# Kernel optimization log

Measured on AMD Instinct MI355X. Metric: run time of the kernel, lower is better.

The kernel has to match this reference:

```python
import jax, jax.numpy as jnp
import numpy as np

N_NODES = 50000
N_EDGES = 800000
N_GRAPHS = 8
BN_EPS = 1e-5


def setup_inputs() -> dict:
    key = jax.random.key(0)
    ks = iter(jax.random.split(key, 40))
    d = {}
    d["x"] = jax.random.normal(next(ks), (N_NODES, 3), dtype=jnp.float32)
    d["edge_index"] = jax.random.randint(next(ks), (2, N_EDGES), 0, N_NODES, dtype=jnp.int32)
    d["batch"] = jnp.sort(jax.random.randint(next(ks), (N_NODES,), 0, N_GRAPHS, dtype=jnp.int32))
    conv_in = [3, 64, 128]  # dense concat widths feeding each GCN layer
    for i, cin in enumerate(conv_in):
        d[f"W{i}"] = jax.random.normal(next(ks), (cin, 64), dtype=jnp.float32) * (1.0 / np.sqrt(cin))
        d[f"b{i}"] = jax.random.normal(next(ks), (64,), dtype=jnp.float32) * 0.05
        d[f"g{i}"] = jax.random.uniform(next(ks), (64,), dtype=jnp.float32) + 0.5
        d[f"beta{i}"] = jax.random.normal(next(ks), (64,), dtype=jnp.float32) * 0.05
        d[f"rm{i}"] = jax.random.normal(next(ks), (64,), dtype=jnp.float32) * 0.05
        d[f"rv{i}"] = jax.random.uniform(next(ks), (64,), dtype=jnp.float32) + 0.5
    def lin(k, i, o):
        return (jax.random.normal(k, (i, o), dtype=jnp.float32) * (1.0 / np.sqrt(i)),)
    d["enc_w0"], = lin(next(ks), 256, 128); d["enc_b0"] = jax.random.normal(next(ks), (128,), jnp.float32) * 0.05
    d["enc_w1"], = lin(next(ks), 128, 64); d["enc_b1"] = jax.random.normal(next(ks), (64,), jnp.float32) * 0.05
    d["dec_w0"], = lin(next(ks), 64, 32); d["dec_b0"] = jax.random.normal(next(ks), (32,), jnp.float32) * 0.05
    d["dec_w1"], = lin(next(ks), 32, 1); d["dec_b1"] = jax.random.normal(next(ks), (1,), jnp.float32) * 0.05
    return d


def reference(x, edge_index, batch,
              W0, b0, g0, beta0, rm0, rv0,
              W1, b1, g1, beta1, rm1, rv1,
              W2, b2, g2, beta2, rm2, rv2,
              enc_w0, enc_b0, enc_w1, enc_b1,
              dec_w0, dec_b0, dec_w1, dec_b1):
    N = x.shape[0]
    loops = jnp.arange(N, dtype=edge_index.dtype)
    src = jnp.concatenate([edge_index[0], loops])  # GCNConv adds self loops
    dst = jnp.concatenate([edge_index[1], loops])
    deg = jax.ops.segment_sum(jnp.ones_like(src, dtype=x.dtype), dst, num_segments=N)
    dinv = jnp.where(deg > 0, jax.lax.rsqrt(deg), 0.0)
    coef = (dinv[src] * dinv[dst])[:, None]  # symmetric normalization per edge

    def conv_bn_relu(h, W, b, g, beta, rm, rv):
        hw = h @ W                                    # [N, 64]
        out = jax.ops.segment_sum(hw[src] * coef, dst, num_segments=N) + b
        out = (out - rm) * (g * jax.lax.rsqrt(rv + BN_EPS)) + beta  # BN eval mode
        return jax.nn.relu(out)

    params = [(W0, b0, g0, beta0, rm0, rv0),
              (W1, b1, g1, beta1, rm1, rv1),
              (W2, b2, g2, beta2, rm2, rv2)]
    prev = []
    h = x
    for p in params:  # dense connectivity: concat all previous concat-outputs
        h = conv_bn_relu(h, *p)
        h = jnp.concatenate(prev + [h], axis=1)
        prev.append(h)

    e = jax.nn.relu(jax.nn.relu(h @ enc_w0 + enc_b0) @ enc_w1 + enc_b1)  # [N, 64]
    counts = jax.ops.segment_sum(jnp.ones((N,), x.dtype), batch, num_segments=N_GRAPHS)
    gfeat = jax.ops.segment_sum(e, batch, num_segments=N_GRAPHS) / jnp.maximum(counts, 1.0)[:, None]
    out = jax.nn.relu(gfeat @ dec_w0 + dec_b0) @ dec_w1 + dec_b1  # [G, 1]
    return out[:, 0]  # torch.squeeze(output, 1) since num_classes == 1
```

## Files before the change

kernel.cpp:

```cpp
#include <hip/hip_runtime.h>
#include <hip/hip_fp16.h>

#define NN 50000
#define NE 800000
#define NG 8
#define BN_EPS 1e-5f
#define NBLK ((NN + 255) / 256)
#define NPART 8
#define HLD 192

typedef __attribute__((ext_vector_type(8))) short bf16x8;
typedef __attribute__((ext_vector_type(4))) float f32x4;

static __device__ __forceinline__ unsigned short f2bf(float f) {
    unsigned int u = __float_as_uint(f);
    unsigned int r = (u + 0x7FFFu + ((u >> 16) & 1u)) >> 16;
    return (unsigned short)r;
}
static __device__ __forceinline__ float bf2f(unsigned short h) {
    return __uint_as_float((unsigned int)h << 16);
}


__global__ __launch_bounds__(256) void count_deg(const int* __restrict__ dst,
                                                 int* __restrict__ degi) {
    int e = blockIdx.x * 256 + threadIdx.x;
    if (e < NE) atomicAdd(&degi[dst[e]], 1);
}

__global__ __launch_bounds__(256) void scan_partial(const int* __restrict__ degi,
                                                    const float* __restrict__ x,
                                                    int* __restrict__ rowptr,
                                                    int* __restrict__ bsum,
                                                    float* __restrict__ dinv,
                                                    float* __restrict__ xs) {
    __shared__ int sh[256];
    const int tid = threadIdx.x;
    const int i = blockIdx.x * 256 + tid;
    int v = (i < NN) ? degi[i] : 0;
    if (i < NN) {
        float di = rsqrtf((float)(v + 1));
        dinv[i] = di;
        xs[i * 3 + 0] = x[i * 3 + 0] * di;
        xs[i * 3 + 1] = x[i * 3 + 1] * di;
        xs[i * 3 + 2] = x[i * 3 + 2] * di;
    }
    sh[tid] = v;
    __syncthreads();
#pragma unroll
    for (int off = 1; off < 256; off <<= 1) {
        int t = (tid >= off) ? sh[tid - off] : 0;
        __syncthreads();
        sh[tid] += t;
        __syncthreads();
    }
    if (i < NN) rowptr[i] = sh[tid] - v;
    if (tid == 255) bsum[blockIdx.x] = sh[255];
}

__global__ __launch_bounds__(256) void scan_bsums(int* __restrict__ bsum) {
    __shared__ int sh[256];
    const int tid = threadIdx.x;
    int v = (tid < NBLK) ? bsum[tid] : 0;
    sh[tid] = v;
    __syncthreads();
#pragma unroll
    for (int off = 1; off < 256; off <<= 1) {
        int t = (tid >= off) ? sh[tid - off] : 0;
        __syncthreads();
        sh[tid] += t;
        __syncthreads();
    }
    if (tid < NBLK) bsum[tid] = sh[tid] - v;
}

__global__ __launch_bounds__(256) void scan_finalize(const int* __restrict__ bsum,
                                                     int* __restrict__ rowptr,
                                                     int* __restrict__ cursor) {
    const int i = blockIdx.x * 256 + threadIdx.x;
    if (i < NN) {
        int r = rowptr[i] + bsum[blockIdx.x];
        rowptr[i] = r;
        cursor[i] = r;
    }
    if (i == 0) rowptr[NN] = NE;
}

__global__ __launch_bounds__(256) void fill_csr(const int* __restrict__ src,
                                                const int* __restrict__ dst,
                                                int* __restrict__ cursor,
                                                unsigned short* __restrict__ esrc16) {
    int e = blockIdx.x * 256 + threadIdx.x;
    if (e < NE) {
        int s = src[e], d = dst[e];
        int p = atomicAdd(&cursor[d], 1);
        esrc16[p] = (unsigned short)s;
    }
}


static __device__ __forceinline__ void pack_one(const float* W, int NOUT, int li,
                                                float v_override, bool use_override,
                                                unsigned short* ph, unsigned short* pl) {
    int j = li & 7;
    int lane = (li >> 3) & 63;
    int rest = li >> 9;
    int NF = NOUT >> 4;
    int f = rest % NF, ks = rest / NF;
    int k = ks * 32 + (lane >> 4) * 8 + j;
    int col = f * 16 + (lane & 15);
    float v = use_override ? v_override : W[k * NOUT + col];
    unsigned short hi = f2bf(v);
    ph[li] = hi;
    pl[li] = f2bf(v - bf2f(hi));
}

__global__ __launch_bounds__(256) void pack_all(
        const float* __restrict__ W1, const float* __restrict__ W2,
        const float* __restrict__ We0, const float* __restrict__ We1,
        unsigned short* __restrict__ Wp1h, unsigned short* __restrict__ Wp1l,
        unsigned short* __restrict__ Wp2h, unsigned short* __restrict__ Wp2l,
        unsigned short* __restrict__ We0h, unsigned short* __restrict__ We0l,
        unsigned short* __restrict__ We1h, unsigned short* __restrict__ We1l) {
    int idx = blockIdx.x * 256 + threadIdx.x;
    if (idx < 4096) {
        pack_one(W1, 64, idx, 0.f, false, Wp1h, Wp1l);
    } else if (idx < 12288) {
        pack_one(W2, 64, idx - 4096, 0.f, false, Wp2h, Wp2l);
    } else if (idx < 36864) {
        int li = idx - 12288;
        int j = li & 7;
        int lane = (li >> 3) & 63;
        int rest = li >> 9;
        int f = rest % 8, ks = rest / 8;
        int k = ks * 32 + (lane >> 4) * 8 + j;
        int col = f * 16 + (lane & 15);
        float v = (k < 64) ? (We0[k * 128 + col] + We0[(k + 64) * 128 + col])
                           : We0[(k + 64) * 128 + col];
        pack_one(nullptr, 128, li, v, true, We0h, We0l);
    } else if (idx < 45056) {
        pack_one(We1, 64, idx - 36864, 0.f, false, We1h, We1l);
    }
}


template<int K>
__global__ __launch_bounds__(256) void mfma_tab(
        const unsigned short* __restrict__ Ahi,
        const unsigned short* __restrict__ Alo, int lda,
        const unsigned short* __restrict__ Bph,
        const unsigned short* __restrict__ Bpl,
        const float* __restrict__ dinv,
        __half* __restrict__ outH) {
    const int wave = threadIdx.x >> 6;
    const int lane = threadIdx.x & 63;
    const int rbase = blockIdx.x * 64 + wave * 16;
    int arow = rbase + (lane & 15);
    if (arow >= NN) arow = NN - 1;
    const int kbase = (lane >> 4) * 8;

    f32x4 acc[4];
#pragma unroll
    for (int f = 0; f < 4; f++) acc[f] = (f32x4){0.f, 0.f, 0.f, 0.f};

    const unsigned short* pa_hi = Ahi + (size_t)arow * lda + kbase;
    const unsigned short* pa_lo = Alo + (size_t)arow * lda + kbase;
    const unsigned short* pb_hi = Bph + lane * 8;
    const unsigned short* pb_lo = Bpl + lane * 8;

#pragma unroll
    for (int ks = 0; ks < K / 32; ks++) {
        bf16x8 ah = *reinterpret_cast<const bf16x8*>(pa_hi + ks * 32);
        bf16x8 al = *reinterpret_cast<const bf16x8*>(pa_lo + ks * 32);
#pragma unroll
        for (int f = 0; f < 4; f++) {
            bf16x8 bh = *reinterpret_cast<const bf16x8*>(pb_hi + (size_t)((ks * 4 + f) * 64) * 8);
            bf16x8 bl = *reinterpret_cast<const bf16x8*>(pb_lo + (size_t)((ks * 4 + f) * 64) * 8);
            acc[f] = __builtin_amdgcn_mfma_f32_16x16x32_bf16(ah, bh, acc[f], 0, 0, 0);
            acc[f] = __builtin_amdgcn_mfma_f32_16x16x32_bf16(ah, bl, acc[f], 0, 0, 0);
            acc[f] = __builtin_amdgcn_mfma_f32_16x16x32_bf16(al, bh, acc[f], 0, 0, 0);
        }
    }

    const int drow0 = rbase + (lane >> 4) * 4;
    const int dcol = lane & 15;
#pragma unroll
    for (int f = 0; f < 4; f++) {
#pragma unroll
        for (int r = 0; r < 4; r++) {
            int row = drow0 + r;
            if (row < NN)
                outH[(size_t)row * 64 + f * 16 + dcol] = __float2half(acc[f][r] * dinv[row]);
        }
    }
}


__global__ __launch_bounds__(256) void enc_fused(
        const unsigned short* __restrict__ Hhi,
        const unsigned short* __restrict__ Hlo,
        const unsigned short* __restrict__ We0h, const unsigned short* __restrict__ We0l,
        const float* __restrict__ b0,
        const unsigned short* __restrict__ We1h, const unsigned short* __restrict__ We1l,
        const float* __restrict__ b1,
        const int* __restrict__ batch,
        float* __restrict__ gfeat_part) {
    __shared__ float ldsT[4][16][133];
    __shared__ float pool[NG][64];
    const int tid = threadIdx.x;
    const int wave = tid >> 6;
    const int lane = tid & 63;
    const int rbase = blockIdx.x * 64 + wave * 16;

    for (int i = tid; i < NG * 64; i += 256) ((float*)pool)[i] = 0.0f;

    int arow = rbase + (lane & 15);
    if (arow >= NN) arow = NN - 1;
    const int kbase = (lane >> 4) * 8;
    f32x4 acc[8];
#pragma unroll
    for (int f = 0; f < 8; f++) acc[f] = (f32x4){0.f, 0.f, 0.f, 0.f};

    const unsigned short* pa_hi = Hhi + (size_t)arow * HLD + kbase;
    const unsigned short* pa_lo = Hlo + (size_t)arow * HLD + kbase;
#pragma unroll
    for (int ks = 0; ks < 6; ks++) {
        bf16x8 ah = *reinterpret_cast<const bf16x8*>(pa_hi + ks * 32);
        bf16x8 al = *reinterpret_cast<const bf16x8*>(pa_lo + ks * 32);
#pragma unroll
        for (int f = 0; f < 8; f++) {
            bf16x8 bh = *reinterpret_cast<const bf16x8*>(We0h + (size_t)(((ks * 8 + f) * 64 + lane)) * 8);
            bf16x8 bl = *reinterpret_cast<const bf16x8*>(We0l + (size_t)(((ks * 8 + f) * 64 + lane)) * 8);
            acc[f] = __builtin_amdgcn_mfma_f32_16x16x32_bf16(ah, bh, acc[f], 0, 0, 0);
            acc[f] = __builtin_amdgcn_mfma_f32_16x16x32_bf16(ah, bl, acc[f], 0, 0, 0);
            acc[f] = __builtin_amdgcn_mfma_f32_16x16x32_bf16(al, bh, acc[f], 0, 0, 0);
        }
    }

    const int lrow0 = (lane >> 4) * 4;
    const int dcol = lane & 15;
#pragma unroll
    for (int f = 0; f < 8; f++) {
#pragma unroll
        for (int r = 0; r < 4; r++) {
            float v = fmaxf(acc[f][r] + b0[f * 16 + dcol], 0.0f);
            ldsT[wave][lrow0 + r][f * 16 + dcol] = v;
        }
    }
    __syncthreads();

    f32x4 acc2[4];
#pragma unroll
    for (int f = 0; f < 4; f++) acc2[f] = (f32x4){0.f, 0.f, 0.f, 0.f};

    const int trow = lane & 15;
#pragma unroll
    for (int ks = 0; ks < 4; ks++) {
        bf16x8 ah, al;
#pragma unroll
        for (int j = 0; j < 8; j++) {
            float tv = ldsT[wave][trow][ks * 32 + (lane >> 4) * 8 + j];
            unsigned short hi = f2bf(tv);
            ah[j] = (short)hi;
            al[j] = (short)f2bf(tv - bf2f(hi));
        }
#pragma unroll
        for (int f = 0; f < 4; f++) {
            bf16x8 bh = *reinterpret_cast<const bf16x8*>(We1h + (size_t)(((ks * 4 + f) * 64 + lane)) * 8);
            bf16x8 bl = *reinterpret_cast<const bf16x8*>(We1l + (size_t)(((ks * 4 + f) * 64 + lane)) * 8);
            acc2[f] = __builtin_amdgcn_mfma_f32_16x16x32_bf16(ah, bh, acc2[f], 0, 0, 0);
            acc2[f] = __builtin_amdgcn_mfma_f32_16x16x32_bf16(ah, bl, acc2[f], 0, 0, 0);
            acc2[f] = __builtin_amdgcn_mfma_f32_16x16x32_bf16(al, bh, acc2[f], 0, 0, 0);
        }
    }

#pragma unroll
    for (int r = 0; r < 4; r++) {
        int row = rbase + lrow0 + r;
        if (row < NN) {
            int g = batch[row];
#pragma unroll
            for (int f = 0; f < 4; f++) {
                int col = f * 16 + dcol;
                float v = fmaxf(acc2[f][r] + b1[col], 0.0f);
                atomicAdd(&pool[g][col], v);
            }
        }
    }
    __syncthreads();

    const int p = blockIdx.x & (NPART - 1);
    for (int i = tid; i < NG * 64; i += 256)
        atomicAdd(&gfeat_part[p * NG * 64 + i], ((float*)pool)[i]);
}


__global__ __launch_bounds__(256) void agg_x3(
        const float* __restrict__ xs,
        const int* __restrict__ rowptr,
        const unsigned short* __restrict__ esrc16,
        const float* __restrict__ dinv,
        float* __restrict__ ax) {
    const int i = blockIdx.x * 256 + threadIdx.x;
    if (i >= NN) return;
    float a0 = xs[i * 3 + 0];
    float a1 = xs[i * 3 + 1];
    float a2 = xs[i * 3 + 2];
    const int beg = rowptr[i], end = rowptr[i + 1];
    int e = beg;
    for (; e + 3 < end; e += 4) {
        int s0 = esrc16[e], s1 = esrc16[e + 1], s2 = esrc16[e + 2], s3 = esrc16[e + 3];
        a0 += xs[s0 * 3 + 0] + xs[s1 * 3 + 0] + xs[s2 * 3 + 0] + xs[s3 * 3 + 0];
        a1 += xs[s0 * 3 + 1] + xs[s1 * 3 + 1] + xs[s2 * 3 + 1] + xs[s3 * 3 + 1];
        a2 += xs[s0 * 3 + 2] + xs[s1 * 3 + 2] + xs[s2 * 3 + 2] + xs[s3 * 3 + 2];
    }
    for (; e < end; e++) {
        int s = esrc16[e];
        a0 += xs[s * 3 + 0];
        a1 += xs[s * 3 + 1];
        a2 += xs[s * 3 + 2];
    }
    const float di = dinv[i];
    ax[i * 3 + 0] = a0 * di;
    ax[i * 3 + 1] = a1 * di;
    ax[i * 3 + 2] = a2 * di;
}


__global__ __launch_bounds__(256) void l0_bn_relu(
        const float* __restrict__ ax, const float* __restrict__ W0,
        const float* __restrict__ b, const float* __restrict__ g,
        const float* __restrict__ beta, const float* __restrict__ rm,
        const float* __restrict__ rv,
        unsigned short* __restrict__ Hhi, unsigned short* __restrict__ Hlo) {
    const int t = blockIdx.x * 256 + threadIdx.x;
    const int row = t >> 6;
    const int ch = t & 63;
    if (row >= NN) return;
    float a0 = ax[row * 3 + 0], a1 = ax[row * 3 + 1], a2 = ax[row * 3 + 2];
    float v = a0 * W0[0 * 64 + ch] + a1 * W0[1 * 64 + ch] + a2 * W0[2 * 64 + ch] + b[ch];
    float sc = g[ch] * rsqrtf(rv[ch] + BN_EPS);
    v = (v - rm[ch]) * sc + beta[ch];
    v = fmaxf(v, 0.0f);
    unsigned short hi = f2bf(v);
    Hhi[(size_t)row * HLD + ch] = hi;
    Hlo[(size_t)row * HLD + ch] = f2bf(v - bf2f(hi));
}


__global__ __launch_bounds__(256) void gather_bn_relu(
        const __half2* __restrict__ tab2,
        const int* __restrict__ rowptr,
        const unsigned short* __restrict__ esrc16,
        const float* __restrict__ dinv,
        const float* __restrict__ b, const float* __restrict__ g,
        const float* __restrict__ beta, const float* __restrict__ rm,
        const float* __restrict__ rv,
        unsigned short* __restrict__ Hhi, unsigned short* __restrict__ Hlo, int cbase) {
    const int wid = (blockIdx.x * 256 + threadIdx.x) >> 6;
    const int lane = threadIdx.x & 63;
    const int c2 = lane & 31;
    const int grp = lane >> 5;
    if (wid >= NN) return;
    const int beg = rowptr[wid], end = rowptr[wid + 1];
    float a0 = 0.0f, a1 = 0.0f;
    int e = beg + grp;
    for (; e + 6 < end; e += 8) {
        int s0 = esrc16[e], s1 = esrc16[e + 2], s2 = esrc16[e + 4], s3 = esrc16[e + 6];
        float2 f0 = __half22float2(tab2[(size_t)s0 * 32 + c2]);
        float2 f1 = __half22float2(tab2[(size_t)s1 * 32 + c2]);
        float2 f2 = __half22float2(tab2[(size_t)s2 * 32 + c2]);
        float2 f3 = __half22float2(tab2[(size_t)s3 * 32 + c2]);
        a0 += (f0.x + f1.x) + (f2.x + f3.x);
        a1 += (f0.y + f1.y) + (f2.y + f3.y);
    }
    for (; e < end; e += 2) {
        float2 f = __half22float2(tab2[(size_t)esrc16[e] * 32 + c2]);
        a0 += f.x;
        a1 += f.y;
    }
    a0 += __shfl_xor(a0, 32, 64);
    a1 += __shfl_xor(a1, 32, 64);
    float2 fs = __half22float2(tab2[(size_t)wid * 32 + c2]);
    a0 += fs.x;
    a1 += fs.y;
    const float di = dinv[wid];
    a0 *= di;
    a1 *= di;
    const int ch0 = 2 * c2, ch1 = 2 * c2 + 1;
    float v0 = (a0 + b[ch0] - rm[ch0]) * (g[ch0] * rsqrtf(rv[ch0] + BN_EPS)) + beta[ch0];
    float v1 = (a1 + b[ch1] - rm[ch1]) * (g[ch1] * rsqrtf(rv[ch1] + BN_EPS)) + beta[ch1];
    v0 = fmaxf(v0, 0.0f);
    v1 = fmaxf(v1, 0.0f);
    if (grp == 0) {
        unsigned short h0 = f2bf(v0), h1 = f2bf(v1);
        unsigned short l0 = f2bf(v0 - bf2f(h0)), l1 = f2bf(v1 - bf2f(h1));
        size_t o = (size_t)wid * HLD + cbase + ch0;
        *reinterpret_cast<unsigned int*>(&Hhi[o]) = (unsigned int)h0 | ((unsigned int)h1 << 16);
        *reinterpret_cast<unsigned int*>(&Hlo[o]) = (unsigned int)l0 | ((unsigned int)l1 << 16);
    }
}


__global__ __launch_bounds__(256) void dec_kernel(
        const float* __restrict__ gfeat_part, const int* __restrict__ batch,
        const float* __restrict__ w0, const float* __restrict__ b0,
        const float* __restrict__ w1, const float* __restrict__ b1,
        float* __restrict__ out) {
    __shared__ float mg[NG][64];
    __shared__ float mc[NG];
    __shared__ float t1[NG][32];
    const int tid = threadIdx.x;
    for (int idx = tid; idx < NG * 64; idx += 256) {
        float s = 0.0f;
#pragma unroll
        for (int p = 0; p < NPART; p++) s += gfeat_part[p * NG * 64 + idx];
        mg[idx >> 6][idx & 63] = s;
    }
    if (tid < NG) {
        int lo = 0, hi = NN;
        while (lo < hi) { int m = (lo + hi) >> 1; if (batch[m] < tid) lo = m + 1; else hi = m; }
        int s0 = lo;
        lo = 0; hi = NN;
        while (lo < hi) { int m = (lo + hi) >> 1; if (batch[m] < tid + 1) lo = m + 1; else hi = m; }
        mc[tid] = (float)(lo - s0);
    }
    __syncthreads();
    const int g = tid >> 5, c = tid & 31;
    float inv = 1.0f / fmaxf(mc[g], 1.0f);
    float acc = b0[c];
    for (int k = 0; k < 64; k++)
        acc = fmaf(mg[g][k] * inv, w0[k * 32 + c], acc);
    t1[g][c] = fmaxf(acc, 0.0f);
    __syncthreads();
    if (tid < NG) {
        float o = b1[0];
        for (int c2 = 0; c2 < 32; c2++) o = fmaf(t1[tid][c2], w1[c2], o);
        out[tid] = o;
    }
}


extern "C" void kernel_launch(void* const* d_in, const int* in_sizes, int n_in,
                              void* d_out, int out_size, void* d_ws, size_t ws_size,
                              hipStream_t stream) {
    const float* x      = (const float*)d_in[0];
    const int*   ei     = (const int*)d_in[1];
    const int*   batch  = (const int*)d_in[2];
    const float* W0     = (const float*)d_in[3];
    const float* b0     = (const float*)d_in[4];
    const float* g0     = (const float*)d_in[5];
    const float* beta0  = (const float*)d_in[6];
    const float* rm0    = (const float*)d_in[7];
    const float* rv0    = (const float*)d_in[8];
    const float* W1     = (const float*)d_in[9];
    const float* b1     = (const float*)d_in[10];
    const float* g1     = (const float*)d_in[11];
    const float* beta1  = (const float*)d_in[12];
    const float* rm1    = (const float*)d_in[13];
    const float* rv1    = (const float*)d_in[14];
    const float* W2     = (const float*)d_in[15];
    const float* b2     = (const float*)d_in[16];
    const float* g2     = (const float*)d_in[17];
    const float* beta2  = (const float*)d_in[18];
    const float* rm2    = (const float*)d_in[19];
    const float* rv2    = (const float*)d_in[20];
    const float* enc_w0 = (const float*)d_in[21];
    const float* enc_b0 = (const float*)d_in[22];
    const float* enc_w1 = (const float*)d_in[23];
    const float* enc_b1 = (const float*)d_in[24];
    const float* dec_w0 = (const float*)d_in[25];
    const float* dec_b0 = (const float*)d_in[26];
    const float* dec_w1 = (const float*)d_in[27];
    const float* dec_b1 = (const float*)d_in[28];

    const int* esrc = ei;
    const int* edst = ei + NE;

    char* wsb = (char*)d_ws;
    unsigned short* Hhi = (unsigned short*)wsb;
    unsigned short* Hlo = Hhi + (size_t)NN * HLD;
    int*   degi   = (int*)(Hlo + (size_t)NN * HLD);
    int*   rowptr = degi + NN;
    int*   cursor = rowptr + NN + 1;
    unsigned short* esrc16 = (unsigned short*)(cursor + NN);
    __half* tabh  = (__half*)(esrc16 + NE);
    float* dinv   = (float*)(tabh + (size_t)NN * 64);
    float* xs     = dinv + NN;
    float* ax     = xs + (size_t)NN * 3;
    float* gfeat_part = ax + (size_t)NN * 3;
    int*   bsum   = (int*)(gfeat_part + NPART * NG * 64);
    unsigned short* wp = (unsigned short*)(bsum + NBLK);
    unsigned short* Wp1h = wp;              unsigned short* Wp1l = Wp1h + 64 * 64;
    unsigned short* Wp2h = Wp1l + 64 * 64;  unsigned short* Wp2l = Wp2h + 128 * 64;
    unsigned short* We0h = Wp2l + 128 * 64; unsigned short* We0l = We0h + 192 * 128;
    unsigned short* We1h = We0l + 192 * 128;unsigned short* We1l = We1h + 128 * 64;

    hipMemsetAsync(gfeat_part, 0, NPART * NG * 64 * sizeof(float), stream);
    hipMemsetAsync(degi, 0, NN * sizeof(int), stream);

    count_deg<<<(NE + 255) / 256, 256, 0, stream>>>(edst, degi);
    scan_partial<<<NBLK, 256, 0, stream>>>(degi, x, rowptr, bsum, dinv, xs);
    scan_bsums<<<1, 256, 0, stream>>>(bsum);
    scan_finalize<<<NBLK, 256, 0, stream>>>(bsum, rowptr, cursor);
    fill_csr<<<(NE + 255) / 256, 256, 0, stream>>>(esrc, edst, cursor, esrc16);

    pack_all<<<(45056 + 255) / 256, 256, 0, stream>>>(W1, W2, enc_w0, enc_w1,
                                                      Wp1h, Wp1l, Wp2h, Wp2l,
                                                      We0h, We0l, We1h, We1l);

    const int GRID_MFMA = (NN + 63) / 64;
    const int GRID_64   = (NN * 64 + 255) / 256;

    agg_x3<<<NBLK, 256, 0, stream>>>(xs, rowptr, esrc16, dinv, ax);
    l0_bn_relu<<<GRID_64, 256, 0, stream>>>(ax, W0, b0, g0, beta0, rm0, rv0, Hhi, Hlo);

    mfma_tab<64><<<GRID_MFMA, 256, 0, stream>>>(Hhi, Hlo, HLD, Wp1h, Wp1l, dinv, tabh);
    gather_bn_relu<<<GRID_64, 256, 0, stream>>>((const __half2*)tabh, rowptr, esrc16, dinv,
                                                b1, g1, beta1, rm1, rv1, Hhi, Hlo, 64);

    mfma_tab<128><<<GRID_MFMA, 256, 0, stream>>>(Hhi, Hlo, HLD, Wp2h, Wp2l, dinv, tabh);
    gather_bn_relu<<<GRID_64, 256, 0, stream>>>((const __half2*)tabh, rowptr, esrc16, dinv,
                                                b2, g2, beta2, rm2, rv2, Hhi, Hlo, 128);

    enc_fused<<<GRID_MFMA, 256, 0, stream>>>(Hhi, Hlo, We0h, We0l, enc_b0,
                                             We1h, We1l, enc_b1, batch, gfeat_part);

    dec_kernel<<<1, 256, 0, stream>>>(gfeat_part, batch, dec_w0, dec_b0, dec_w1, dec_b1, (float*)d_out);
}
```

Measured before the change: 261.4 us.

## Preload MFMA weight fragments and use a block-uniform fast path for graph pooling

In mfma_tab, all B-weight and A-row fragments are loaded into registers before the MFMA loop, and a min-blocks-per-CU hint of 2 is added. In enc_fused, the next K-slice of We0 fragments is double-buffered in registers and all We1 fragments are preloaded. When every row of a block belongs to the same graph, pooling now uses a wave shuffle reduction plus one global atomic per column, in place of per-element LDS atomics. The aim is to hide global-load latency and reduce atomic traffic, at the cost of higher register pressure, which could cause spills under the launch-bounds hint.

Measured after the change: 244.2 us. 6.6% less time.

```diff
diff --git a/kernel.cpp b/kernel.cpp
--- a/kernel.cpp
+++ b/kernel.cpp
@@ -145,13 +145,14 @@
 
 
 template<int K>
-__global__ __launch_bounds__(256) void mfma_tab(
+__global__ __launch_bounds__(256, 2) void mfma_tab(
         const unsigned short* __restrict__ Ahi,
         const unsigned short* __restrict__ Alo, int lda,
         const unsigned short* __restrict__ Bph,
         const unsigned short* __restrict__ Bpl,
         const float* __restrict__ dinv,
         __half* __restrict__ outH) {
+    constexpr int KS = K / 32;
     const int wave = threadIdx.x >> 6;
     const int lane = threadIdx.x & 63;
     const int rbase = blockIdx.x * 64 + wave * 16;
@@ -159,28 +160,36 @@
     if (arow >= NN) arow = NN - 1;
     const int kbase = (lane >> 4) * 8;
 
-    f32x4 acc[4];
-#pragma unroll
-    for (int f = 0; f < 4; f++) acc[f] = (f32x4){0.f, 0.f, 0.f, 0.f};
+    bf16x8 bh[KS][4], bl[KS][4];
+#pragma unroll
+    for (int ks = 0; ks < KS; ks++)
+#pragma unroll
+        for (int f = 0; f < 4; f++) {
+            bh[ks][f] = *reinterpret_cast<const bf16x8*>(Bph + (size_t)((ks * 4 + f) * 64 + lane) * 8);
+            bl[ks][f] = *reinterpret_cast<const bf16x8*>(Bpl + (size_t)((ks * 4 + f) * 64 + lane) * 8);
+        }
 
     const unsigned short* pa_hi = Ahi + (size_t)arow * lda + kbase;
     const unsigned short* pa_lo = Alo + (size_t)arow * lda + kbase;
-    const unsigned short* pb_hi = Bph + lane * 8;
-    const unsigned short* pb_lo = Bpl + lane * 8;
-
-#pragma unroll
-    for (int ks = 0; ks < K / 32; ks++) {
-        bf16x8 ah = *reinterpret_cast<const bf16x8*>(pa_hi + ks * 32);
-        bf16x8 al = *reinterpret_cast<const bf16x8*>(pa_lo + ks * 32);
+    bf16x8 ah[KS], al[KS];
+#pragma unroll
+    for (int ks = 0; ks < KS; ks++) {
+        ah[ks] = *reinterpret_cast<const bf16x8*>(pa_hi + ks * 32);
+        al[ks] = *reinterpret_cast<const bf16x8*>(pa_lo + ks * 32);
+    }
+
+    f32x4 acc[4];
+#pragma unroll
+    for (int f = 0; f < 4; f++) acc[f] = (f32x4){0.f, 0.f, 0.f, 0.f};
+
+#pragma unroll
+    for (int ks = 0; ks < KS; ks++)
 #pragma unroll
         for (int f = 0; f < 4; f++) {
-            bf16x8 bh = *reinterpret_cast<const bf16x8*>(pb_hi + (size_t)((ks * 4 + f) * 64) * 8);
-            bf16x8 bl = *reinterpret_cast<const bf16x8*>(pb_lo + (size_t)((ks * 4 + f) * 64) * 8);
-            acc[f] = __builtin_amdgcn_mfma_f32_16x16x32_bf16(ah, bh, acc[f], 0, 0, 0);
-            acc[f] = __builtin_amdgcn_mfma_f32_16x16x32_bf16(ah, bl, acc[f], 0, 0, 0);
-            acc[f] = __builtin_amdgcn_mfma_f32_16x16x32_bf16(al, bh, acc[f], 0, 0, 0);
-        }
-    }
+            acc[f] = __builtin_amdgcn_mfma_f32_16x16x32_bf16(ah[ks], bh[ks][f], acc[f], 0, 0, 0);
+            acc[f] = __builtin_amdgcn_mfma_f32_16x16x32_bf16(ah[ks], bl[ks][f], acc[f], 0, 0, 0);
+            acc[f] = __builtin_amdgcn_mfma_f32_16x16x32_bf16(al[ks], bh[ks][f], acc[f], 0, 0, 0);
+        }
 
     const int drow0 = rbase + (lane >> 4) * 4;
     const int dcol = lane & 15;
@@ -196,7 +205,7 @@
 }
 
 
-__global__ __launch_bounds__(256) void enc_fused(
+__global__ __launch_bounds__(256, 2) void enc_fused(
         const unsigned short* __restrict__ Hhi,
         const unsigned short* __restrict__ Hlo,
         const unsigned short* __restrict__ We0h, const unsigned short* __restrict__ We0l,
@@ -206,14 +215,13 @@
         const int* __restrict__ batch,
         float* __restrict__ gfeat_part) {
     __shared__ float ldsT[4][16][133];
+    __shared__ float poolw[4][64];
     __shared__ float pool[NG][64];
     const int tid = threadIdx.x;
     const int wave = tid >> 6;
     const int lane = tid & 63;
     const int rbase = blockIdx.x * 64 + wave * 16;
 
-    for (int i = tid; i < NG * 64; i += 256) ((float*)pool)[i] = 0.0f;
-
     int arow = rbase + (lane & 15);
     if (arow >= NN) arow = NN - 1;
     const int kbase = (lane >> 4) * 8;
@@ -223,17 +231,33 @@
 
     const unsigned short* pa_hi = Hhi + (size_t)arow * HLD + kbase;
     const unsigned short* pa_lo = Hlo + (size_t)arow * HLD + kbase;
+
+    bf16x8 cbh[8], cbl[8], nbh[8], nbl[8];
+#pragma unroll
+    for (int f = 0; f < 8; f++) {
+        cbh[f] = *reinterpret_cast<const bf16x8*>(We0h + (size_t)(f * 64 + lane) * 8);
+        cbl[f] = *reinterpret_cast<const bf16x8*>(We0l + (size_t)(f * 64 + lane) * 8);
+    }
 #pragma unroll
     for (int ks = 0; ks < 6; ks++) {
+        if (ks < 5) {
+#pragma unroll
+            for (int f = 0; f < 8; f++) {
+                nbh[f] = *reinterpret_cast<const bf16x8*>(We0h + (size_t)(((ks + 1) * 8 + f) * 64 + lane) * 8);
+                nbl[f] = *reinterpret_cast<const bf16x8*>(We0l + (size_t)(((ks + 1) * 8 + f) * 64 + lane) * 8);
+            }
+        }
         bf16x8 ah = *reinterpret_cast<const bf16x8*>(pa_hi + ks * 32);
         bf16x8 al = *reinterpret_cast<const bf16x8*>(pa_lo + ks * 32);
 #pragma unroll
         for (int f = 0; f < 8; f++) {
-            bf16x8 bh = *reinterpret_cast<const bf16x8*>(We0h + (size_t)(((ks * 8 + f) * 64 + lane)) * 8);
-            bf16x8 bl = *reinterpret_cast<const bf16x8*>(We0l + (size_t)(((ks * 8 + f) * 64 + lane)) * 8);
-            acc[f] = __builtin_amdgcn_mfma_f32_16x16x32_bf16(ah, bh, acc[f], 0, 0, 0);
-            acc[f] = __builtin_amdgcn_mfma_f32_16x16x32_bf16(ah, bl, acc[f], 0, 0, 0);
-            acc[f] = __builtin_amdgcn_mfma_f32_16x16x32_bf16(al, bh, acc[f], 0, 0, 0);
+            acc[f] = __builtin_amdgcn_mfma_f32_16x16x32_bf16(ah, cbh[f], acc[f], 0, 0, 0);
+            acc[f] = __builtin_amdgcn_mfma_f32_16x16x32_bf16(ah, cbl[f], acc[f], 0, 0, 0);
+            acc[f] = __builtin_amdgcn_mfma_f32_16x16x32_bf16(al, cbh[f], acc[f], 0, 0, 0);
+        }
+        if (ks < 5) {
+#pragma unroll
+            for (int f = 0; f < 8; f++) { cbh[f] = nbh[f]; cbl[f] = nbl[f]; }
         }
     }
 
@@ -248,6 +272,15 @@
         }
     }
     __syncthreads();
+
+    bf16x8 wbh[4][4], wbl[4][4];
+#pragma unroll
+    for (int ks = 0; ks < 4; ks++)
+#pragma unroll
+        for (int f = 0; f < 4; f++) {
+            wbh[ks][f] = *reinterpret_cast<const bf16x8*>(We1h + (size_t)((ks * 4 + f) * 64 + lane) * 8);
+            wbl[ks][f] = *reinterpret_cast<const bf16x8*>(We1l + (size_t)((ks * 4 + f) * 64 + lane) * 8);
+        }
 
     f32x4 acc2[4];
 #pragma unroll
@@ -266,32 +299,58 @@
         }
 #pragma unroll
         for (int f = 0; f < 4; f++) {
-            bf16x8 bh = *reinterpret_cast<const bf16x8*>(We1h + (size_t)(((ks * 4 + f) * 64 + lane)) * 8);
-            bf16x8 bl = *reinterpret_cast<const bf16x8*>(We1l + (size_t)(((ks * 4 + f) * 64 + lane)) * 8);
-            acc2[f] = __builtin_amdgcn_mfma_f32_16x16x32_bf16(ah, bh, acc2[f], 0, 0, 0);
-            acc2[f] = __builtin_amdgcn_mfma_f32_16x16x32_bf16(ah, bl, acc2[f], 0, 0, 0);
-            acc2[f] = __builtin_amdgcn_mfma_f32_16x16x32_bf16(al, bh, acc2[f], 0, 0, 0);
-        }
-    }
-
-#pragma unroll
-    for (int r = 0; r < 4; r++) {
-        int row = rbase + lrow0 + r;
-        if (row < NN) {
-            int g = batch[row];
-#pragma unroll
-            for (int f = 0; f < 4; f++) {
-                int col = f * 16 + dcol;
-                float v = fmaxf(acc2[f][r] + b1[col], 0.0f);
-                atomicAdd(&pool[g][col], v);
+            acc2[f] = __builtin_amdgcn_mfma_f32_16x16x32_bf16(ah, wbh[ks][f], acc2[f], 0, 0, 0);
+            acc2[f] = __builtin_amdgcn_mfma_f32_16x16x32_bf16(ah, wbl[ks][f], acc2[f], 0, 0, 0);
+            acc2[f] = __builtin_amdgcn_mfma_f32_16x16x32_bf16(al, wbh[ks][f], acc2[f], 0, 0, 0);
+        }
+    }
+
+    float vout[4][4];
+#pragma unroll
+    for (int f = 0; f < 4; f++)
+#pragma unroll
+        for (int r = 0; r < 4; r++) {
+            int row = rbase + lrow0 + r;
+            vout[f][r] = (row < NN) ? fmaxf(acc2[f][r] + b1[f * 16 + dcol], 0.0f) : 0.0f;
+        }
+
+    const int blk_row0 = blockIdx.x * 64;
+    const int blk_rowN = min(blk_row0 + 63, NN - 1);
+    const int g0 = batch[blk_row0];
+    const int p = blockIdx.x & (NPART - 1);
+
+    if (g0 == batch[blk_rowN]) {
+#pragma unroll
+        for (int f = 0; f < 4; f++) {
+            float s = (vout[f][0] + vout[f][1]) + (vout[f][2] + vout[f][3]);
+            s += __shfl_xor(s, 16, 64);
+            s += __shfl_xor(s, 32, 64);
+            if ((lane >> 4) == 0) poolw[wave][f * 16 + dcol] = s;
+        }
+        __syncthreads();
+        if (tid < 64) {
+            float s = (poolw[0][tid] + poolw[1][tid]) + (poolw[2][tid] + poolw[3][tid]);
+            atomicAdd(&gfeat_part[(p * NG + g0) * 64 + tid], s);
+        }
+    } else {
+        for (int i = tid; i < NG * 64; i += 256) ((float*)pool)[i] = 0.0f;
+        __syncthreads();
+#pragma unroll
+        for (int r = 0; r < 4; r++) {
+            int row = rbase + lrow0 + r;
+            if (row < NN) {
+                int g = batch[row];
+#pragma unroll
+                for (int f = 0; f < 4; f++)
+                    atomicAdd(&pool[g][f * 16 + dcol], vout[f][r]);
             }
         }
-    }
-    __syncthreads();
-
-    const int p = blockIdx.x & (NPART - 1);
-    for (int i = tid; i < NG * 64; i += 256)
-        atomicAdd(&gfeat_part[p * NG * 64 + i], ((float*)pool)[i]);
+        __syncthreads();
+        for (int i = tid; i < NG * 64; i += 256) {
+            float s = ((float*)pool)[i];
+            if (s != 0.0f) atomicAdd(&gfeat_part[p * NG * 64 + i], s);
+        }
+    }
 }
 
 
```
